# Kernel tuning notes

Measured on AMD Instinct MI355X. Metric: run time of the kernel, lower is better.

The kernel has to match this reference:

```python
import jax, jax.numpy as jnp
import numpy as np

D = 1024
B, S = 4, 4096


def setup_inputs() -> dict:
    key = jax.random.key(0)
    ks = jax.random.split(key, 5)
    scale = 1.0 / np.sqrt(D)  # ~ torch Linear init magnitude
    return {
        "x": jax.random.normal(ks[0], (B, S, D), dtype=jnp.float32),
        "Wa": jax.random.normal(ks[1], (D, D), dtype=jnp.float32) * scale,
        "Wb": jax.random.normal(ks[2], (D, D), dtype=jnp.float32) * scale,
        "Wc": jax.random.normal(ks[3], (D, D), dtype=jnp.float32) * scale,
        "Wd": jax.random.normal(ks[4], (D, D), dtype=jnp.float32) * scale,
    }


def reference(x, Wa, Wb, Wc, Wd):
    # torch nn.Linear(bias=False): y = x @ W.T, W is [out, in]
    A = jax.nn.relu(jnp.einsum("bsd,ed->bse", x, Wa))
    Bm = jax.nn.relu(jnp.einsum("bsd,ed->bse", x, Wb))
    C = jax.nn.relu(jnp.einsum("bsd,ed->bse", x, Wc))
    cmp_matrix = jnp.einsum("bse,bte->bst", A, Bm)  # [B,S,S] unnormalized scores
    out = jnp.einsum("bst,bte->bse", cmp_matrix, C)
    return jax.nn.relu(jnp.einsum("bsd,ed->bse", out, Wd))
```

## Files before the change

### kernel.cpp

```cpp
#include <hip/hip_runtime.h>
#include <hip/hip_bf16.h>

#define D_ 1024
#define B_ 4
#define S_ 4096

typedef __attribute__((ext_vector_type(8))) short bf16x8;
typedef __attribute__((ext_vector_type(4))) float f32x4;
typedef __attribute__((ext_vector_type(4))) unsigned int u32x4;
typedef __attribute__((ext_vector_type(4))) unsigned short u16x4;

__device__ __forceinline__ unsigned short f2bf(float f) {
    unsigned int u = __builtin_bit_cast(unsigned int, f);
    u = u + 0x7fffu + ((u >> 16) & 1u);
    return (unsigned short)(u >> 16);
}
__device__ __forceinline__ unsigned int pk2(float a, float b) {
    return (unsigned int)f2bf(a) | ((unsigned int)f2bf(b) << 16);
}
__device__ __forceinline__ float bf2f(unsigned short h) {
    unsigned int u = ((unsigned int)h) << 16;
    return __builtin_bit_cast(float, u);
}
__device__ __forceinline__ void gload16(const void* g, void* l) {
    __builtin_amdgcn_global_load_lds(
        (const __attribute__((address_space(1))) void*)g,
        (__attribute__((address_space(3))) void*)l, 16, 0, 0);
}

__device__ __forceinline__ void conv8(const float* s, unsigned short* d, size_t j) {
    f32x4 v0 = *(const f32x4*)(s + j);
    f32x4 v1 = *(const f32x4*)(s + j + 4);
    u32x4 o;
    o[0] = pk2(v0[0], v0[1]);
    o[1] = pk2(v0[2], v0[3]);
    o[2] = pk2(v1[0], v1[1]);
    o[3] = pk2(v1[2], v1[3]);
    *(u32x4*)(d + j) = o;
}

__global__ __launch_bounds__(256)
void conv_all(const float* __restrict__ x, const float* __restrict__ Wb,
              const float* __restrict__ Wc,
              unsigned short* __restrict__ xb, unsigned short* __restrict__ wbb,
              unsigned short* __restrict__ wcb, int n8x, int n8w) {
    int i = blockIdx.x * blockDim.x + threadIdx.x;
    const int stride = gridDim.x * blockDim.x;
    const int ntot = n8x + 2 * n8w;
    for (; i < ntot; i += stride) {
        if (i < n8x)                conv8(x,  xb,  (size_t)i * 8);
        else if (i < n8x + n8w)     conv8(Wb, wbb, (size_t)(i - n8x) * 8);
        else                        conv8(Wc, wcb, (size_t)(i - n8x - n8w) * 8);
    }
}

__global__ __launch_bounds__(256)
void reduce_convw(const unsigned short* __restrict__ P, unsigned short* __restrict__ E,
                  const float* __restrict__ Wd, const float* __restrict__ Wa,
                  unsigned short* __restrict__ wdb, unsigned short* __restrict__ wab,
                  int n8e, int n8w) {
    int t = blockIdx.x * blockDim.x + threadIdx.x;
    const int stride = gridDim.x * blockDim.x;
    const int DD = D_ * D_;
    const int ntot = n8e + 2 * n8w;
    for (; t < ntot; t += stride) {
        if (t < n8e) {
            size_t idx = (size_t)t * 8;
            int b = (int)(idx / DD);
            size_t i = idx % DD;
            float s[8];
#pragma unroll
            for (int k = 0; k < 8; ++k) s[k] = 0.f;
#pragma unroll
            for (int seg = 0; seg < 4; ++seg) {
                const unsigned short* p = P + (size_t)(b * 4 + seg) * DD + i;
                u16x4 v0 = *(const u16x4*)p;
                u16x4 v1 = *(const u16x4*)(p + 4);
#pragma unroll
                for (int k = 0; k < 4; ++k) { s[k] += bf2f(v0[k]); s[4 + k] += bf2f(v1[k]); }
            }
            u16x4 o0, o1;
#pragma unroll
            for (int k = 0; k < 4; ++k) { o0[k] = f2bf(s[k]); o1[k] = f2bf(s[4 + k]); }
            *(u16x4*)(E + idx) = o0;
            *(u16x4*)(E + idx + 4) = o1;
        } else if (t < n8e + n8w) {
            conv8(Wd, wdb, (size_t)(t - n8e) * 8);
        } else {
            conv8(Wa, wab, (size_t)(t - n8e - n8w) * 8);
        }
    }
}

#define BM 128
#define BN 128
#define BK 64
#define NTHR 256

template<bool OUT_F32, bool TRANS, bool RELU>
__global__ __launch_bounds__(NTHR)
void gemm_nt(const unsigned short* __restrict__ Ap, const unsigned short* __restrict__ Bp,
             void* __restrict__ Op, int M, int N, int K, int klen, int split,
             long long sA, long long sB, long long sO)
{
    __shared__ char lds_a[BM * BK * 2];
    __shared__ char lds_b[BN * BK * 2];

    const int tid   = threadIdx.x;
    const int bz    = blockIdx.z;
    const int batch = bz / split;
    const int k0    = (bz % split) * klen;
    const int bm    = blockIdx.y * BM;
    const int bn    = blockIdx.x * BN;

    const unsigned short* Abase = Ap + (size_t)batch * sA + (size_t)bm * K;
    const unsigned short* Bbase = Bp + (size_t)batch * sB + (size_t)bn * K;

    const int lane = tid & 63;
    const int wave = tid >> 6;
    const int wm   = (wave >> 1) * 64;
    const int wn   = (wave & 1) * 64;
    const int l16  = lane & 15;
    const int lhi  = lane >> 4;

    const int schnk = (lane & 7) ^ (lane >> 3);
    const char* gA0 = (const char*)(Abase + (size_t)(wave * 32 + (lane >> 3)) * K) + schnk * 16;
    const char* gB0 = (const char*)(Bbase + (size_t)(wave * 32 + (lane >> 3)) * K) + schnk * 16;
    char* lA0 = lds_a + wave * 4096;
    char* lB0 = lds_b + wave * 4096;

    f32x4 acc[4][4];
#pragma unroll
    for (int i = 0; i < 4; ++i)
#pragma unroll
        for (int j = 0; j < 4; ++j)
            acc[i][j] = (f32x4){0.f, 0.f, 0.f, 0.f};

    for (int kt = k0; kt < k0 + klen; kt += BK) {
#pragma unroll
        for (int p = 0; p < 4; ++p)
            gload16(gA0 + ((size_t)p * 8 * K + kt) * 2, lA0 + p * 1024);
#pragma unroll
        for (int p = 0; p < 4; ++p)
            gload16(gB0 + ((size_t)p * 8 * K + kt) * 2, lB0 + p * 1024);
        __syncthreads();
#pragma unroll
        for (int kk = 0; kk < BK / 32; ++kk) {
            bf16x8 af[4], bfr[4];
#pragma unroll
            for (int i = 0; i < 4; ++i) {
                int row = wm + i * 16 + l16;
                int byt = (row * 128 + kk * 64 + lhi * 16) ^ ((row & 7) << 4);
                af[i] = *(const bf16x8*)(lds_a + byt);
            }
#pragma unroll
            for (int j = 0; j < 4; ++j) {
                int row = wn + j * 16 + l16;
                int byt = (row * 128 + kk * 64 + lhi * 16) ^ ((row & 7) << 4);
                bfr[j] = *(const bf16x8*)(lds_b + byt);
            }
#pragma unroll
            for (int i = 0; i < 4; ++i)
#pragma unroll
                for (int j = 0; j < 4; ++j)
                    acc[i][j] = __builtin_amdgcn_mfma_f32_16x16x32_bf16(af[i], bfr[j], acc[i][j], 0, 0, 0);
        }
        __syncthreads();
    }

    const size_t obase = (size_t)bz * (size_t)sO;
    if constexpr (!TRANS) {
#pragma unroll
        for (int i = 0; i < 4; ++i) {
            const int m0 = bm + wm + i * 16 + lhi * 4;
#pragma unroll
            for (int j = 0; j < 4; ++j) {
                const int n = bn + wn + j * 16 + l16;
#pragma unroll
                for (int r = 0; r < 4; ++r) {
                    float v = acc[i][j][r];
                    if constexpr (RELU) v = fmaxf(v, 0.f);
                    size_t addr = obase + (size_t)(m0 + r) * N + n;
                    if constexpr (OUT_F32) ((float*)Op)[addr] = v;
                    else ((unsigned short*)Op)[addr] = f2bf(v);
                }
            }
        }
    } else {
#pragma unroll
        for (int i = 0; i < 4; ++i) {
            const int m0 = bm + wm + i * 16 + lhi * 4;
#pragma unroll
            for (int j = 0; j < 4; ++j) {
                const int n = bn + wn + j * 16 + l16;
                u16x4 h;
#pragma unroll
                for (int r = 0; r < 4; ++r) {
                    float v = acc[i][j][r];
                    if constexpr (RELU) v = fmaxf(v, 0.f);
                    h[r] = f2bf(v);
                }
                *(u16x4*)((unsigned short*)Op + obase + (size_t)n * M + m0) = h;
            }
        }
    }
}

#define CTILE 65536
#define CBOFF 32768

template<bool OUT_F32, bool TRANS, bool RELU>
__global__ __launch_bounds__(512, 2)
void gemm256(const unsigned short* __restrict__ Ap, const unsigned short* __restrict__ Bp,
             void* __restrict__ Op, int M, int N, int K, int klen, int split,
             long long sA, long long sB, long long sO)
{
    __shared__ char lds[131072];
    const int tid  = threadIdx.x;
    const int wave = tid >> 6;
    const int lane = tid & 63;

    const int gx = gridDim.x, gy = gridDim.y;
    const int f   = blockIdx.x + gx * (blockIdx.y + gy * blockIdx.z);
    const int nwg = gx * gy * (int)gridDim.z;
    const int s   = (f & 7) * (nwg >> 3) + (f >> 3);
    const int lx  = s % gx;
    const int lyz = s / gx;
    const int ly  = lyz % gy;
    const int lz  = lyz / gy;

    const int batch = lz / split;
    const int k0    = (lz % split) * klen;
    const int bm    = ly * 256;
    const int bn    = lx * 256;

    const int wm  = (wave >> 2) * 128;
    const int wn  = (wave & 3) * 64;
    const int l16 = lane & 15, lhi = lane >> 4;

    const unsigned short* Abase = Ap + (size_t)batch * sA + (size_t)bm * K;
    const unsigned short* Bbase = Bp + (size_t)batch * sB + (size_t)bn * K;
    const int srow  = lane >> 3;
    const int schnk = (lane & 7) ^ srow;
    const size_t K2 = (size_t)K * 2;
    const char* gA = (const char*)Abase + (size_t)srow * K2 + (size_t)schnk * 16 + (size_t)k0 * 2;
    const char* gB = (const char*)Bbase + (size_t)srow * K2 + (size_t)schnk * 16 + (size_t)k0 * 2;

    const int lxor = (l16 & 7) << 4;
    const int aX = (wm + l16) * 128 + lhi * 16;
    const int bX = (wn + l16) * 128 + lhi * 16;
    const char* aB00 = lds + 0 * CTILE + ((aX + 0 * 64) ^ lxor);
    const char* aB01 = lds + 0 * CTILE + ((aX + 1 * 64) ^ lxor);
    const char* aB10 = lds + 1 * CTILE + ((aX + 0 * 64) ^ lxor);
    const char* aB11 = lds + 1 * CTILE + ((aX + 1 * 64) ^ lxor);
    const char* bB00 = lds + 0 * CTILE + CBOFF + ((bX + 0 * 64) ^ lxor);
    const char* bB01 = lds + 0 * CTILE + CBOFF + ((bX + 1 * 64) ^ lxor);
    const char* bB10 = lds + 1 * CTILE + CBOFF + ((bX + 0 * 64) ^ lxor);
    const char* bB11 = lds + 1 * CTILE + CBOFF + ((bX + 1 * 64) ^ lxor);

    f32x4 acc[8][4];
#pragma unroll
    for (int i = 0; i < 8; ++i)
#pragma unroll
        for (int j = 0; j < 4; ++j)
            acc[i][j] = (f32x4){0.f, 0.f, 0.f, 0.f};

    bf16x8 a[4][2], b0[2][2], b1[2][2];

    auto stageA2 = [&](int c, int t, int h) {
#pragma unroll
        for (int p = 0; p < 2; ++p)
            gload16(gA + (size_t)t * 128 + (size_t)(h * 128 + wave * 16 + p * 8) * K2,
                    lds + c * CTILE + h * 16384 + wave * 2048 + p * 1024);
    };
    auto stageB2 = [&](int c, int t, int h) {
#pragma unroll
        for (int p = 0; p < 2; ++p)
            gload16(gB + (size_t)t * 128 + (size_t)(h * 128 + wave * 16 + p * 8) * K2,
                    lds + c * CTILE + CBOFF + h * 16384 + wave * 2048 + p * 1024);
    };
    auto ldAh = [&](int c, int mh, int lo) {
        const char* base0 = c ? aB10 : aB00;
        const char* base1 = c ? aB11 : aB01;
#pragma unroll
        for (int i4 = 0; i4 < 2; ++i4) {
            const int imm = (mh * 64 + (lo + i4) * 16) * 128;
            a[lo + i4][0] = *(const bf16x8*)(base0 + imm);
            a[lo + i4][1] = *(const bf16x8*)(base1 + imm);
        }
    };
    auto ldBh = [&](int c, int nh, bf16x8 (&bb)[2][2], int j2) {
        const char* base0 = c ? bB10 : bB00;
        const char* base1 = c ? bB11 : bB01;
        const int imm = (nh * 32 + j2 * 16) * 128;
        bb[j2][0] = *(const bf16x8*)(base0 + imm);
        bb[j2][1] = *(const bf16x8*)(base1 + imm);
    };
    auto ldB = [&](int c, int nh, bf16x8 (&bb)[2][2]) {
        ldBh(c, nh, bb, 0); ldBh(c, nh, bb, 1);
    };
    auto mmH = [&](int mh, int nh, bf16x8 (&bb)[2][2], int lo) {
        __builtin_amdgcn_s_setprio(1);
#pragma unroll
        for (int i4 = 0; i4 < 2; ++i4)
#pragma unroll
            for (int j2 = 0; j2 < 2; ++j2)
#pragma unroll
                for (int kk = 0; kk < 2; ++kk)
                    acc[mh * 4 + lo + i4][nh * 2 + j2] = __builtin_amdgcn_mfma_f32_16x16x32_bf16(
                        a[lo + i4][kk], bb[j2][kk], acc[mh * 4 + lo + i4][nh * 2 + j2], 0, 0, 0);
        __builtin_amdgcn_s_setprio(0);
    };
    auto mm = [&](int mh, int nh, bf16x8 (&bb)[2][2]) { mmH(mh, nh, bb, 0); mmH(mh, nh, bb, 2); };

#define BAR()   __builtin_amdgcn_s_barrier()
#define LGKM0() asm volatile("s_waitcnt lgkmcnt(0)" ::: "memory")
#define VM2()   asm volatile("s_waitcnt vmcnt(2)" ::: "memory")
#define VM4()   asm volatile("s_waitcnt vmcnt(4)" ::: "memory")
#define VM6()   asm volatile("s_waitcnt vmcnt(6)" ::: "memory")

    const int NT = klen / 64;
    stageB2(0, 0, 0); stageB2(0, 0, 1); stageA2(0, 0, 0); stageA2(0, 0, 1);
    stageB2(1, 1, 0); stageB2(1, 1, 1); stageA2(1, 1, 0);
    VM6();
    BAR();
    ldB(0, 0, b0); ldAh(0, 0, 0); ldAh(0, 0, 2);

    for (int itr = 0; itr < NT / 2; ++itr) {
        const int t1  = 2 * itr + 1;
        const int tp0 = (2 * itr + 2) % NT;
        const int tp1 = (2 * itr + 3) % NT;
        LGKM0(); mmH(0, 0, b0, 0);
        ldBh(0, 1, b1, 0);
        mmH(0, 0, b0, 2);
        ldBh(0, 1, b1, 1); stageA2(1, t1, 1);
        BAR();
        LGKM0(); mmH(0, 1, b1, 0);
        ldAh(0, 1, 0);
        mmH(0, 1, b1, 2);
        ldAh(0, 1, 2); VM4();
        BAR();
        LGKM0(); mm(1, 0, b0);
        ldB(1, 0, b0); stageB2(0, tp0, 0); VM2();
        BAR();
        LGKM0(); mmH(1, 1, b1, 0);
        ldAh(1, 0, 0);
        mmH(1, 1, b1, 2);
        ldAh(1, 0, 2); stageB2(0, tp0, 1); stageA2(0, tp0, 0);
        BAR();
        LGKM0(); mmH(0, 0, b0, 0);
        ldBh(1, 1, b1, 0);
        mmH(0, 0, b0, 2);
        ldBh(1, 1, b1, 1); stageA2(0, tp0, 1);
        BAR();
        LGKM0(); mmH(0, 1, b1, 0);
        ldAh(1, 1, 0);
        mmH(0, 1, b1, 2);
        ldAh(1, 1, 2); VM4();
        BAR();
        LGKM0(); mm(1, 0, b0);
        ldB(0, 0, b0); stageB2(1, tp1, 0); VM2();
        BAR();
        LGKM0(); mmH(1, 1, b1, 0);
        ldAh(0, 0, 0);
        mmH(1, 1, b1, 2);
        ldAh(0, 0, 2); stageB2(1, tp1, 1); stageA2(1, tp1, 0);
        BAR();
    }
    asm volatile("s_waitcnt vmcnt(0)" ::: "memory");

    const size_t obase = (size_t)lz * (size_t)sO;
    if constexpr (!TRANS) {
#pragma unroll
        for (int i = 0; i < 8; ++i) {
            const int m0 = bm + wm + i * 16 + lhi * 4;
#pragma unroll
            for (int j = 0; j < 4; ++j) {
                const int n = bn + wn + j * 16 + l16;
#pragma unroll
                for (int r = 0; r < 4; ++r) {
                    float v = acc[i][j][r];
                    if constexpr (RELU) v = fmaxf(v, 0.f);
                    size_t addr = obase + (size_t)(m0 + r) * N + n;
                    if constexpr (OUT_F32) ((float*)Op)[addr] = v;
                    else ((unsigned short*)Op)[addr] = f2bf(v);
                }
            }
        }
    } else {
#pragma unroll
        for (int i = 0; i < 8; ++i) {
            const int m0 = bm + wm + i * 16 + lhi * 4;
#pragma unroll
            for (int j = 0; j < 4; ++j) {
                const int n = bn + wn + j * 16 + l16;
                u16x4 h;
#pragma unroll
                for (int r = 0; r < 4; ++r) {
                    float v = acc[i][j][r];
                    if constexpr (RELU) v = fmaxf(v, 0.f);
                    h[r] = f2bf(v);
                }
                *(u16x4*)((unsigned short*)Op + obase + (size_t)n * M + m0) = h;
            }
        }
    }
#undef BAR
#undef LGKM0
#undef VM2
#undef VM4
#undef VM6
}

template<bool OUT_F32, bool TRANS, bool RELU>
__global__ __launch_bounds__(1024, 4)
void gemm256w16(const unsigned short* __restrict__ Ap, const unsigned short* __restrict__ Bp,
                void* __restrict__ Op, int M, int N, int K, int klen, int split,
                long long sA, long long sB, long long sO)
{
    __shared__ char lds[131072];
    const int tid  = threadIdx.x;
    const int wave = tid >> 6;
    const int lane = tid & 63;

    const int gx = gridDim.x, gy = gridDim.y;
    const int f   = blockIdx.x + gx * (blockIdx.y + gy * blockIdx.z);
    const int nwg = gx * gy * (int)gridDim.z;
    const int s   = (f & 7) * (nwg >> 3) + (f >> 3);
    const int lx  = s % gx;
    const int lyz = s / gx;
    const int ly  = lyz % gy;
    const int lz  = lyz / gy;

    const int batch = lz / split;
    const int k0    = (lz % split) * klen;
    const int bm    = ly * 256;
    const int bn    = lx * 256;

    const int wm  = (wave >> 2) * 64;
    const int wn  = (wave & 3) * 64;
    const int l16 = lane & 15, lhi = lane >> 4;

    const unsigned short* Abase = Ap + (size_t)batch * sA + (size_t)bm * K;
    const unsigned short* Bbase = Bp + (size_t)batch * sB + (size_t)bn * K;
    const int srowB = tid >> 3;
    const int schnk = (lane & 7) ^ (lane >> 3);
    const size_t K2 = (size_t)K * 2;
    const char* gA = (const char*)Abase + (size_t)srowB * K2 + (size_t)schnk * 16 + (size_t)k0 * 2;
    const char* gB = (const char*)Bbase + (size_t)srowB * K2 + (size_t)schnk * 16 + (size_t)k0 * 2;

    const int lxor = (l16 & 7) << 4;
    const int aX = (wm + l16) * 128 + lhi * 16;
    const int bX = (wn + l16) * 128 + lhi * 16;
    const char* aB00 = lds + 0 * CTILE + ((aX + 0 * 64) ^ lxor);
    const char* aB01 = lds + 0 * CTILE + ((aX + 1 * 64) ^ lxor);
    const char* aB10 = lds + 1 * CTILE + ((aX + 0 * 64) ^ lxor);
    const char* aB11 = lds + 1 * CTILE + ((aX + 1 * 64) ^ lxor);
    const char* bB00 = lds + 0 * CTILE + CBOFF + ((bX + 0 * 64) ^ lxor);
    const char* bB01 = lds + 0 * CTILE + CBOFF + ((bX + 1 * 64) ^ lxor);
    const char* bB10 = lds + 1 * CTILE + CBOFF + ((bX + 0 * 64) ^ lxor);
    const char* bB11 = lds + 1 * CTILE + CBOFF + ((bX + 1 * 64) ^ lxor);

    f32x4 acc[4][4];
#pragma unroll
    for (int i = 0; i < 4; ++i)
#pragma unroll
        for (int j = 0; j < 4; ++j)
            acc[i][j] = (f32x4){0.f, 0.f, 0.f, 0.f};

    bf16x8 a[2][2], b0[2][2], b1[2][2];

    auto stageA2 = [&](int c, int t, int h) {
        gload16(gA + (size_t)t * 128 + (size_t)(h * 128) * K2,
                lds + c * CTILE + h * 16384 + wave * 1024);
    };
    auto stageB2 = [&](int c, int t, int h) {
        gload16(gB + (size_t)t * 128 + (size_t)(h * 128) * K2,
                lds + c * CTILE + CBOFF + h * 16384 + wave * 1024);
    };
    auto ldAh = [&](int c, int mh, int q) {
        const char* base0 = c ? aB10 : aB00;
        const char* base1 = c ? aB11 : aB01;
        const int imm = (mh * 32 + q * 16) * 128;
        a[q][0] = *(const bf16x8*)(base0 + imm);
        a[q][1] = *(const bf16x8*)(base1 + imm);
    };
    auto ldBh = [&](int c, int nh, bf16x8 (&bb)[2][2], int j2) {
        const char* base0 = c ? bB10 : bB00;
        const char* base1 = c ? bB11 : bB01;
        const int imm = (nh * 32 + j2 * 16) * 128;
        bb[j2][0] = *(const bf16x8*)(base0 + imm);
        bb[j2][1] = *(const bf16x8*)(base1 + imm);
    };
    auto ldB = [&](int c, int nh, bf16x8 (&bb)[2][2]) {
        ldBh(c, nh, bb, 0); ldBh(c, nh, bb, 1);
    };
    auto mmH = [&](int mh, int nh, bf16x8 (&bb)[2][2], int q) {
        __builtin_amdgcn_s_setprio(1);
#pragma unroll
        for (int j2 = 0; j2 < 2; ++j2)
#pragma unroll
            for (int kk = 0; kk < 2; ++kk)
                acc[mh * 2 + q][nh * 2 + j2] = __builtin_amdgcn_mfma_f32_16x16x32_bf16(
                    a[q][kk], bb[j2][kk], acc[mh * 2 + q][nh * 2 + j2], 0, 0, 0);
        __builtin_amdgcn_s_setprio(0);
    };
    auto mm = [&](int mh, int nh, bf16x8 (&bb)[2][2]) { mmH(mh, nh, bb, 0); mmH(mh, nh, bb, 1); };

#define BAR()   __builtin_amdgcn_s_barrier()
#define LGKM0() asm volatile("s_waitcnt lgkmcnt(0)" ::: "memory")
#define VM1()   asm volatile("s_waitcnt vmcnt(1)" ::: "memory")
#define VM2()   asm volatile("s_waitcnt vmcnt(2)" ::: "memory")
#define VM3()   asm volatile("s_waitcnt vmcnt(3)" ::: "memory")

    const int NT = klen / 64;
    stageB2(0, 0, 0); stageB2(0, 0, 1); stageA2(0, 0, 0); stageA2(0, 0, 1);
    stageB2(1, 1, 0); stageB2(1, 1, 1); stageA2(1, 1, 0);
    VM3();
    BAR();
    ldB(0, 0, b0); ldAh(0, 0, 0); ldAh(0, 0, 1);

    for (int itr = 0; itr < NT / 2; ++itr) {
        const int t1  = 2 * itr + 1;
        const int tp0 = (2 * itr + 2) % NT;
        const int tp1 = (2 * itr + 3) % NT;
        LGKM0(); mmH(0, 0, b0, 0);
        ldBh(0, 1, b1, 0);
        mmH(0, 0, b0, 1);
        ldBh(0, 1, b1, 1); stageA2(1, t1, 1);
        BAR();
        LGKM0(); mmH(0, 1, b1, 0);
        ldAh(0, 1, 0);
        mmH(0, 1, b1, 1);
        ldAh(0, 1, 1); VM2();
        BAR();
        LGKM0(); mm(1, 0, b0);
        ldB(1, 0, b0); stageB2(0, tp0, 0); VM1();
        BAR();
        LGKM0(); mmH(1, 1, b1, 0);
        ldAh(1, 0, 0);
        mmH(1, 1, b1, 1);
        ldAh(1, 0, 1); stageB2(0, tp0, 1); stageA2(0, tp0, 0);
        BAR();
        LGKM0(); mmH(0, 0, b0, 0);
        ldBh(1, 1, b1, 0);
        mmH(0, 0, b0, 1);
        ldBh(1, 1, b1, 1); stageA2(0, tp0, 1);
        BAR();
        LGKM0(); mmH(0, 1, b1, 0);
        ldAh(1, 1, 0);
        mmH(0, 1, b1, 1);
        ldAh(1, 1, 1); VM2();
        BAR();
        LGKM0(); mm(1, 0, b0);
        ldB(0, 0, b0); stageB2(1, tp1, 0); VM1();
        BAR();
        LGKM0(); mmH(1, 1, b1, 0);
        ldAh(0, 0, 0);
        mmH(1, 1, b1, 1);
        ldAh(0, 0, 1); stageB2(1, tp1, 1); stageA2(1, tp1, 0);
        BAR();
    }
    asm volatile("s_waitcnt vmcnt(0)" ::: "memory");

    const size_t obase = (size_t)lz * (size_t)sO;
    if constexpr (!TRANS) {
#pragma unroll
        for (int i = 0; i < 4; ++i) {
            const int m0 = bm + wm + i * 16 + lhi * 4;
#pragma unroll
            for (int j = 0; j < 4; ++j) {
                const int n = bn + wn + j * 16 + l16;
#pragma unroll
                for (int r = 0; r < 4; ++r) {
                    float v = acc[i][j][r];
                    if constexpr (RELU) v = fmaxf(v, 0.f);
                    size_t addr = obase + (size_t)(m0 + r) * N + n;
                    if constexpr (OUT_F32) ((float*)Op)[addr] = v;
                    else ((unsigned short*)Op)[addr] = f2bf(v);
                }
            }
        }
    } else {
#pragma unroll
        for (int i = 0; i < 4; ++i) {
            const int m0 = bm + wm + i * 16 + lhi * 4;
#pragma unroll
            for (int j = 0; j < 4; ++j) {
                const int n = bn + wn + j * 16 + l16;
                u16x4 h;
#pragma unroll
                for (int r = 0; r < 4; ++r) {
                    float v = acc[i][j][r];
                    if constexpr (RELU) v = fmaxf(v, 0.f);
                    h[r] = f2bf(v);
                }
                *(u16x4*)((unsigned short*)Op + obase + (size_t)n * M + m0) = h;
            }
        }
    }
#undef BAR
#undef LGKM0
#undef VM1
#undef VM2
#undef VM3
}

extern "C" void kernel_launch(void* const* d_in, const int* in_sizes, int n_in,
                              void* d_out, int out_size, void* d_ws, size_t ws_size,
                              hipStream_t stream) {
    (void)in_sizes; (void)n_in; (void)out_size; (void)ws_size;
    const float* x  = (const float*)d_in[0];
    const float* Wa = (const float*)d_in[1];
    const float* Wb = (const float*)d_in[2];
    const float* Wc = (const float*)d_in[3];
    const float* Wd = (const float*)d_in[4];

    const long long SD  = (long long)S_ * D_;
    const long long DD2 = (long long)D_ * D_;
    const size_t MB = 1024 * 1024;

    unsigned short* BC    = (unsigned short*)d_ws;
    unsigned short* Enorm = (unsigned short*)d_ws;
    unsigned short* Ao    = (unsigned short*)d_ws;
    unsigned short* Ft    = (unsigned short*)((char*)d_ws + 32 * MB);
    unsigned short* Wdb   = (unsigned short*)((char*)d_ws + 40 * MB);
    unsigned short* Wab   = (unsigned short*)((char*)d_ws + 42 * MB);
    char* ob = (char*)d_out;
    unsigned short* xb  = (unsigned short*)ob;
    unsigned short* Pp  = (unsigned short*)(ob + 32 * MB);
    unsigned short* Wbb = (unsigned short*)(ob + 56 * MB);
    unsigned short* Wcb = (unsigned short*)(ob + 58 * MB);

    dim3 blk256(256, 1, 1);
    dim3 blk512(512, 1, 1);
    dim3 blk1024(1024, 1, 1);
    dim3 gBC(2048 / 256, S_ / 256, B_);
    dim3 gE(D_ / 256, D_ / 256, B_ * 4);
    dim3 gS(D_ / 256, S_ / 256, B_);
    dim3 gF(D_ / BN, D_ / BM, B_);

    const int n8x = (B_ * S_ * D_) / 8;
    const int n8w = (D_ * D_) / 8;
    const int n8e = (B_ * D_ * D_) / 8;

    conv_all<<<2048, blk256, 0, stream>>>(x, Wb, Wc, xb, Wbb, Wcb, n8x, n8w);
    gemm256w16<false, true,  true ><<<gBC, blk1024, 0, stream>>>(xb, Wbb, BC, S_, 2048, D_, D_, 1, SD, 0, 2 * SD);
    gemm256w16<false, false, false><<<gE, blk1024, 0, stream>>>(BC, BC + SD, Pp, D_, D_, S_, S_ / 4, 4, 2 * SD, 2 * SD, DD2);
    reduce_convw<<<1024, blk256, 0, stream>>>(Pp, Enorm, Wd, Wa, Wdb, Wab, n8e, n8w);
    gemm_nt<false, true,  false><<<gF, blk256, 0, stream>>>(Enorm, Wdb, Ft, D_, D_, D_, D_, 1, DD2, 0, DD2);
    gemm256<false, false, true ><<<gS, blk512, 0, stream>>>(xb, Wab, Ao, S_, D_, D_, D_, 1, SD, 0, SD);
    gemm256<true,  false, true ><<<gS, blk512, 0, stream>>>(Ao, Ft, (float*)d_out, S_, D_, D_, D_, 1, SD, DD2, SD);
}
```

Baseline: 241.3 us.

## Use 512-thread 256x256 GEMM with 128x64 per-wave tiles for BC and E

Replaces the 1024-thread (16-wave) 256x256 GEMM with an 8-wave variant in which each wave computes a 128x64 sub-tile, doubling accumulators and A-fragment registers per wave. Global-to-LDS staging issues two loads per wave per half-tile, and the pipelined schedule is re-sequenced with fewer barriers and adjusted vmcnt waits. The aim is more MFMA work per LDS fragment load and less barrier overhead. The cost is much higher register pressure, which limits occupancy and could cause spills.

```diff
diff --git a/kernel.cpp b/kernel.cpp
--- a/kernel.cpp
+++ b/kernel.cpp
@@ -413,10 +413,10 @@
 }
 
 template<bool OUT_F32, bool TRANS, bool RELU>
-__global__ __launch_bounds__(1024, 4)
-void gemm256w16(const unsigned short* __restrict__ Ap, const unsigned short* __restrict__ Bp,
-                void* __restrict__ Op, int M, int N, int K, int klen, int split,
-                long long sA, long long sB, long long sO)
+__global__ __launch_bounds__(512, 2)
+void gemm256p6(const unsigned short* __restrict__ Ap, const unsigned short* __restrict__ Bp,
+               void* __restrict__ Op, int M, int N, int K, int klen, int split,
+               long long sA, long long sB, long long sO)
 {
     __shared__ char lds[131072];
     const int tid  = threadIdx.x;
@@ -437,17 +437,17 @@
     const int bm    = ly * 256;
     const int bn    = lx * 256;
 
-    const int wm  = (wave >> 2) * 64;
+    const int wm  = (wave >> 2) * 128;
     const int wn  = (wave & 3) * 64;
     const int l16 = lane & 15, lhi = lane >> 4;
 
     const unsigned short* Abase = Ap + (size_t)batch * sA + (size_t)bm * K;
     const unsigned short* Bbase = Bp + (size_t)batch * sB + (size_t)bn * K;
-    const int srowB = tid >> 3;
-    const int schnk = (lane & 7) ^ (lane >> 3);
+    const int srow  = lane >> 3;
+    const int schnk = (lane & 7) ^ srow;
     const size_t K2 = (size_t)K * 2;
-    const char* gA = (const char*)Abase + (size_t)srowB * K2 + (size_t)schnk * 16 + (size_t)k0 * 2;
-    const char* gB = (const char*)Bbase + (size_t)srowB * K2 + (size_t)schnk * 16 + (size_t)k0 * 2;
+    const char* gA = (const char*)Abase + (size_t)srow * K2 + (size_t)schnk * 16 + (size_t)k0 * 2;
+    const char* gB = (const char*)Bbase + (size_t)srow * K2 + (size_t)schnk * 16 + (size_t)k0 * 2;
 
     const int lxor = (l16 & 7) << 4;
     const int aX = (wm + l16) * 128 + lhi * 16;
@@ -461,29 +461,36 @@
     const char* bB10 = lds + 1 * CTILE + CBOFF + ((bX + 0 * 64) ^ lxor);
     const char* bB11 = lds + 1 * CTILE + CBOFF + ((bX + 1 * 64) ^ lxor);
 
-    f32x4 acc[4][4];
-#pragma unroll
-    for (int i = 0; i < 4; ++i)
+    f32x4 acc[8][4];
+#pragma unroll
+    for (int i = 0; i < 8; ++i)
 #pragma unroll
         for (int j = 0; j < 4; ++j)
             acc[i][j] = (f32x4){0.f, 0.f, 0.f, 0.f};
 
-    bf16x8 a[2][2], b0[2][2], b1[2][2];
+    bf16x8 a[4][2], b0[2][2], b1[2][2];
 
     auto stageA2 = [&](int c, int t, int h) {
-        gload16(gA + (size_t)t * 128 + (size_t)(h * 128) * K2,
-                lds + c * CTILE + h * 16384 + wave * 1024);
+#pragma unroll
+        for (int p = 0; p < 2; ++p)
+            gload16(gA + (size_t)t * 128 + (size_t)(h * 128 + wave * 16 + p * 8) * K2,
+                    lds + c * CTILE + h * 16384 + wave * 2048 + p * 1024);
     };
     auto stageB2 = [&](int c, int t, int h) {
-        gload16(gB + (size_t)t * 128 + (size_t)(h * 128) * K2,
-                lds + c * CTILE + CBOFF + h * 16384 + wave * 1024);
-    };
-    auto ldAh = [&](int c, int mh, int q) {
+#pragma unroll
+        for (int p = 0; p < 2; ++p)
+            gload16(gB + (size_t)t * 128 + (size_t)(h * 128 + wave * 16 + p * 8) * K2,
+                    lds + c * CTILE + CBOFF + h * 16384 + wave * 2048 + p * 1024);
+    };
+    auto ldAh = [&](int c, int mh, int lo) {
         const char* base0 = c ? aB10 : aB00;
         const char* base1 = c ? aB11 : aB01;
-        const int imm = (mh * 32 + q * 16) * 128;
-        a[q][0] = *(const bf16x8*)(base0 + imm);
-        a[q][1] = *(const bf16x8*)(base1 + imm);
+#pragma unroll
+        for (int i4 = 0; i4 < 2; ++i4) {
+            const int imm = (mh * 64 + (lo + i4) * 16) * 128;
+            a[lo + i4][0] = *(const bf16x8*)(base0 + imm);
+            a[lo + i4][1] = *(const bf16x8*)(base1 + imm);
+        }
     };
     auto ldBh = [&](int c, int nh, bf16x8 (&bb)[2][2], int j2) {
         const char* base0 = c ? bB10 : bB00;
@@ -495,30 +502,30 @@
     auto ldB = [&](int c, int nh, bf16x8 (&bb)[2][2]) {
         ldBh(c, nh, bb, 0); ldBh(c, nh, bb, 1);
     };
-    auto mmH = [&](int mh, int nh, bf16x8 (&bb)[2][2], int q) {
+    auto mmH = [&](int mh, int nh, bf16x8 (&bb)[2][2], int lo) {
         __builtin_amdgcn_s_setprio(1);
 #pragma unroll
-        for (int j2 = 0; j2 < 2; ++j2)
-#pragma unroll
-            for (int kk = 0; kk < 2; ++kk)
-                acc[mh * 2 + q][nh * 2 + j2] = __builtin_amdgcn_mfma_f32_16x16x32_bf16(
-                    a[q][kk], bb[j2][kk], acc[mh * 2 + q][nh * 2 + j2], 0, 0, 0);
+        for (int i4 = 0; i4 < 2; ++i4)
+#pragma unroll
+            for (int j2 = 0; j2 < 2; ++j2)
+#pragma unroll
+                for (int kk = 0; kk < 2; ++kk)
+                    acc[mh * 4 + lo + i4][nh * 2 + j2] = __builtin_amdgcn_mfma_f32_16x16x32_bf16(
+                        a[lo + i4][kk], bb[j2][kk], acc[mh * 4 + lo + i4][nh * 2 + j2], 0, 0, 0);
         __builtin_amdgcn_s_setprio(0);
     };
-    auto mm = [&](int mh, int nh, bf16x8 (&bb)[2][2]) { mmH(mh, nh, bb, 0); mmH(mh, nh, bb, 1); };
 
 #define BAR()   __builtin_amdgcn_s_barrier()
 #define LGKM0() asm volatile("s_waitcnt lgkmcnt(0)" ::: "memory")
-#define VM1()   asm volatile("s_waitcnt vmcnt(1)" ::: "memory")
 #define VM2()   asm volatile("s_waitcnt vmcnt(2)" ::: "memory")
-#define VM3()   asm volatile("s_waitcnt vmcnt(3)" ::: "memory")
+#define VM4()   asm volatile("s_waitcnt vmcnt(4)" ::: "memory")
 
     const int NT = klen / 64;
     stageB2(0, 0, 0); stageB2(0, 0, 1); stageA2(0, 0, 0); stageA2(0, 0, 1);
-    stageB2(1, 1, 0); stageB2(1, 1, 1); stageA2(1, 1, 0);
-    VM3();
+    stageB2(1, 1, 0); stageB2(1, 1, 1);
+    VM4();
     BAR();
-    ldB(0, 0, b0); ldAh(0, 0, 0); ldAh(0, 0, 1);
+    ldB(0, 0, b0); ldAh(0, 0, 0); ldAh(0, 0, 2);
 
     for (int itr = 0; itr < NT / 2; ++itr) {
         const int t1  = 2 * itr + 1;
@@ -526,39 +533,35 @@
         const int tp1 = (2 * itr + 3) % NT;
         LGKM0(); mmH(0, 0, b0, 0);
         ldBh(0, 1, b1, 0);
-        mmH(0, 0, b0, 1);
-        ldBh(0, 1, b1, 1); stageA2(1, t1, 1);
+        mmH(0, 0, b0, 2);
+        ldBh(0, 1, b1, 1); stageA2(1, t1, 0); stageA2(1, t1, 1);
         BAR();
         LGKM0(); mmH(0, 1, b1, 0);
         ldAh(0, 1, 0);
-        mmH(0, 1, b1, 1);
-        ldAh(0, 1, 1); VM2();
-        BAR();
-        LGKM0(); mm(1, 0, b0);
-        ldB(1, 0, b0); stageB2(0, tp0, 0); VM1();
-        BAR();
-        LGKM0(); mmH(1, 1, b1, 0);
-        ldAh(1, 0, 0);
-        mmH(1, 1, b1, 1);
-        ldAh(1, 0, 1); stageB2(0, tp0, 1); stageA2(0, tp0, 0);
+        mmH(0, 1, b1, 2);
+        ldAh(0, 1, 2); VM4();
+        BAR();
+        LGKM0(); mmH(1, 0, b0, 0); mmH(1, 0, b0, 2);
+        ldBh(1, 0, b0, 0); ldBh(1, 0, b0, 1);
+        mmH(1, 1, b1, 0); mmH(1, 1, b1, 2);
+        stageB2(0, tp0, 0); stageB2(0, tp0, 1); VM2();
+        ldAh(1, 0, 0); ldAh(1, 0, 2);
         BAR();
         LGKM0(); mmH(0, 0, b0, 0);
         ldBh(1, 1, b1, 0);
-        mmH(0, 0, b0, 1);
-        ldBh(1, 1, b1, 1); stageA2(0, tp0, 1);
+        mmH(0, 0, b0, 2);
+        ldBh(1, 1, b1, 1); stageA2(0, tp0, 0); stageA2(0, tp0, 1);
         BAR();
         LGKM0(); mmH(0, 1, b1, 0);
         ldAh(1, 1, 0);
-        mmH(0, 1, b1, 1);
-        ldAh(1, 1, 1); VM2();
-        BAR();
-        LGKM0(); mm(1, 0, b0);
-        ldB(0, 0, b0); stageB2(1, tp1, 0); VM1();
-        BAR();
-        LGKM0(); mmH(1, 1, b1, 0);
-        ldAh(0, 0, 0);
-        mmH(1, 1, b1, 1);
-        ldAh(0, 0, 1); stageB2(1, tp1, 1); stageA2(1, tp1, 0);
+        mmH(0, 1, b1, 2);
+        ldAh(1, 1, 2); VM4();
+        BAR();
+        LGKM0(); mmH(1, 0, b0, 0); mmH(1, 0, b0, 2);
+        ldBh(0, 0, b0, 0); ldBh(0, 0, b0, 1);
+        mmH(1, 1, b1, 0); mmH(1, 1, b1, 2);
+        stageB2(1, tp1, 0); stageB2(1, tp1, 1); VM2();
+        ldAh(0, 0, 0); ldAh(0, 0, 2);
         BAR();
     }
     asm volatile("s_waitcnt vmcnt(0)" ::: "memory");
@@ -566,7 +569,7 @@
     const size_t obase = (size_t)lz * (size_t)sO;
     if constexpr (!TRANS) {
 #pragma unroll
-        for (int i = 0; i < 4; ++i) {
+        for (int i = 0; i < 8; ++i) {
             const int m0 = bm + wm + i * 16 + lhi * 4;
 #pragma unroll
             for (int j = 0; j < 4; ++j) {
@@ -583,7 +586,7 @@
         }
     } else {
 #pragma unroll
-        for (int i = 0; i < 4; ++i) {
+        for (int i = 0; i < 8; ++i) {
             const int m0 = bm + wm + i * 16 + lhi * 4;
 #pragma unroll
             for (int j = 0; j < 4; ++j) {
@@ -601,9 +604,8 @@
     }
 #undef BAR
 #undef LGKM0
-#undef VM1
 #undef VM2
-#undef VM3
+#undef VM4
 }
 
 extern "C" void kernel_launch(void* const* d_in, const int* in_sizes, int n_in,
@@ -634,7 +636,6 @@
 
     dim3 blk256(256, 1, 1);
     dim3 blk512(512, 1, 1);
-    dim3 blk1024(1024, 1, 1);
     dim3 gBC(2048 / 256, S_ / 256, B_);
     dim3 gE(D_ / 256, D_ / 256, B_ * 4);
     dim3 gS(D_ / 256, S_ / 256, B_);
@@ -645,8 +646,8 @@
     const int n8e = (B_ * D_ * D_) / 8;
 
     conv_all<<<2048, blk256, 0, stream>>>(x, Wb, Wc, xb, Wbb, Wcb, n8x, n8w);
-    gemm256w16<false, true,  true ><<<gBC, blk1024, 0, stream>>>(xb, Wbb, BC, S_, 2048, D_, D_, 1, SD, 0, 2 * SD);
-    gemm256w16<false, false, false><<<gE, blk1024, 0, stream>>>(BC, BC + SD, Pp, D_, D_, S_, S_ / 4, 4, 2 * SD, 2 * SD, DD2);
+    gemm256p6<false, true,  true ><<<gBC, blk512, 0, stream>>>(xb, Wbb, BC, S_, 2048, D_, D_, 1, SD, 0, 2 * SD);
+    gemm256p6<false, false, false><<<gE, blk512, 0, stream>>>(BC, BC + SD, Pp, D_, D_, S_, S_ / 4, 4, 2 * SD, 2 * SD, DD2);
     reduce_convw<<<1024, blk256, 0, stream>>>(Pp, Enorm, Wd, Wa, Wdb, Wab, n8e, n8w);
     gemm_nt<false, true,  false><<<gF, blk256, 0, stream>>>(Enorm, Wdb, Ft, D_, D_, D_, D_, 1, DD2, 0, DD2);
     gemm256<false, false, true ><<<gS, blk512, 0, stream>>>(xb, Wab, Ao, S_, D_, D_, D_, 1, SD, 0, SD);
```

After: 243.2 us. No clear change (+0.8%).
